# Optimization experiments

Measured on AMD Instinct MI355X. Metric: run time of the kernel, lower is better.

The kernel has to match this reference:

```python
import jax, jax.numpy as jnp
import numpy as np
import math

S, D = 8192, 128

def setup_inputs() -> dict:
    key = jax.random.key(0)
    kq, kk, kv = jax.random.split(key, 3)
    return {
        "q": jax.random.normal(kq, (S, D), dtype=jnp.float32),
        "k": jax.random.normal(kk, (S, D), dtype=jnp.float32),
        "v": jax.random.normal(kv, (S, D), dtype=jnp.float32),
    }

def reference(q, k, v):
    # scores: [S, S]; scale by sqrt(d) as in the torch module
    scale = 1.0 / math.sqrt(q.shape[1])
    scores = (q @ k.T) * scale
    attn = jax.nn.softmax(scores, axis=-1)
    return attn @ v
```

## Files before the change

kernel.cpp:

```cpp
#include <hip/hip_runtime.h>
#include <hip/hip_bf16.h>

#define SEQ 8192
#define HD 128
#define BM 256
#define BN 64
#define NQT (SEQ / BM)
#define THREADS 512

typedef __bf16 bf16_t;
typedef __bf16 bf16x2 __attribute__((ext_vector_type(2)));
typedef __bf16 bf16x8 __attribute__((ext_vector_type(8)));
typedef float f32x4 __attribute__((ext_vector_type(4)));
typedef float f32x16 __attribute__((ext_vector_type(16)));
typedef unsigned int u32x4 __attribute__((ext_vector_type(4)));

#if __has_builtin(__builtin_amdgcn_exp2f)
__device__ inline float exp2_fast(float x) { return __builtin_amdgcn_exp2f(x); }
#else
__device__ inline float exp2_fast(float x) { return exp2f(x); }
#endif

__device__ inline void permswap32(unsigned int& a, unsigned int& b) {
#if __has_builtin(__builtin_amdgcn_permlane32_swap)
  auto r = __builtin_amdgcn_permlane32_swap(a, b, false, false);
  a = (unsigned int)r[0];
  b = (unsigned int)r[1];
#else
  asm volatile("v_permlane32_swap_b32 %0, %1" : "+v"(a), "+v"(b));
#endif
}

__device__ inline void load_lds16(const void* g, void* l) {
  __builtin_amdgcn_global_load_lds(
      (const __attribute__((address_space(1))) void*)g,
      (__attribute__((address_space(3))) void*)l, 16, 0, 0);
}

#define BARRIER(N)                                                         \
  do {                                                                     \
    asm volatile("s_waitcnt vmcnt(" #N ") lgkmcnt(0)\n\ts_barrier" ::: "memory"); \
    __builtin_amdgcn_sched_barrier(0);                                     \
  } while (0)

__global__ __launch_bounds__(256) void prep_kernel(const float* __restrict__ K,
                                                   const float* __restrict__ V,
                                                   bf16_t* __restrict__ Kb,
                                                   bf16_t* __restrict__ VT) {
  const int b = (int)blockIdx.x;
  const int tid = (int)threadIdx.x;
  if (b < 256) {
    __shared__ float tile[64][65];
    const int T = b & 127;
    const int d0 = (b >> 7) * 64;
    const int s0 = T * 64;
    const int r = tid >> 2;
    const int c0 = (tid & 3) * 16;
#pragma unroll
    for (int j4 = 0; j4 < 4; ++j4) {
      float4 x = *(const float4*)&V[(size_t)(s0 + r) * HD + d0 + c0 + j4 * 4];
      tile[r][c0 + j4 * 4 + 0] = x.x;
      tile[r][c0 + j4 * 4 + 1] = x.y;
      tile[r][c0 + j4 * 4 + 2] = x.z;
      tile[r][c0 + j4 * 4 + 3] = x.w;
    }
    __syncthreads();
    const int d_l = tid & 63;
    const int kc0 = (tid >> 6) * 2;
#pragma unroll
    for (int k2 = 0; k2 < 2; ++k2) {
      const int kc = kc0 + k2;
      bf16x8 wv;
#pragma unroll
      for (int j = 0; j < 8; ++j) wv[j] = (bf16_t)tile[kc * 8 + j][d_l];
      *(bf16x8*)&VT[((size_t)(T * 8 + kc) * 128 + d0 + d_l) * 8] = wv;
    }
  } else {
    const int base = (b - 256) * 2048 + tid * 8;
    const int row = base >> 7;
    const int c = (base >> 3) & 15;
    const int T = row >> 6;
    const int r = row & 63;
    float4 a = *(const float4*)&K[base];
    float4 cc = *(const float4*)&K[base + 4];
    bf16x8 f;
    f[0] = (bf16_t)a.x; f[1] = (bf16_t)a.y; f[2] = (bf16_t)a.z; f[3] = (bf16_t)a.w;
    f[4] = (bf16_t)cc.x; f[5] = (bf16_t)cc.y; f[6] = (bf16_t)cc.z; f[7] = (bf16_t)cc.w;
    *(bf16x8*)&Kb[((size_t)(T * 16 + c) * 64 + r) * 8] = f;
  }
}

__global__ __launch_bounds__(THREADS, 2) void fattn_kernel(
    const float* __restrict__ Q, const bf16_t* __restrict__ Kb,
    const bf16_t* __restrict__ VT, float* __restrict__ Opart,
    float* __restrict__ Lpart, int kshift, int nit) {
  __shared__ __align__(16) bf16_t kt3[3][16][64][8];
  __shared__ __align__(16) bf16_t vt3[3][8][128][8];

  const int tid = (int)threadIdx.x;
  const int lane = tid & 63;
  const int w = tid >> 6;
  const int h = lane >> 5;
  const int n32 = lane & 31;

  const int qt = (int)blockIdx.x >> kshift;
  const int sp = (int)blockIdx.x & ((1 << kshift) - 1);
  const int qbase = qt * BM;
  const int tile0 = sp * nit;

  const float SC2 = 0.08838834764831845f * 1.4426950408889634f;

  bf16x8 qf[8];
  {
    const float* qp = Q + (size_t)(qbase + w * 32 + n32) * HD + h * 8;
#pragma unroll
    for (int kk = 0; kk < 8; ++kk) {
      float4 a = *(const float4*)(qp + kk * 16);
      float4 b = *(const float4*)(qp + kk * 16 + 4);
      bf16x8 f;
      f[0] = (bf16_t)(a.x * SC2); f[1] = (bf16_t)(a.y * SC2);
      f[2] = (bf16_t)(a.z * SC2); f[3] = (bf16_t)(a.w * SC2);
      f[4] = (bf16_t)(b.x * SC2); f[5] = (bf16_t)(b.y * SC2);
      f[6] = (bf16_t)(b.z * SC2); f[7] = (bf16_t)(b.w * SC2);
      qf[kk] = f;
    }
  }

  f32x16 o_acc[4];
#pragma unroll
  for (int i = 0; i < 4; ++i)
#pragma unroll
    for (int e = 0; e < 16; ++e) o_acc[i][e] = 0.f;
  float l_acc = 0.f;

  bf16x8 paA[4], paB[4];

  const int rr0 = w * 2;
  char* const ktB = (char*)&kt3[0][0][0][0];
  char* const vtB = (char*)&vt3[0][0][0][0];

#define DMA_K(TILE, BUF)                                                   \
  _Pragma("unroll")                                                        \
  for (int t = 0; t < 2; ++t) {                                            \
    const int rr = rr0 + t;                                                \
    load_lds16(Kb + ((size_t)((TILE) * 16 + rr) * 64 + lane) * 8,          \
               ktB + (BUF) * 16384 + rr * 1024);                           \
  }
#define DMA_V(TILE, BUF)                                                   \
  _Pragma("unroll")                                                        \
  for (int t = 0; t < 2; ++t) {                                            \
    const int rr = rr0 + t;                                                \
    load_lds16(VT + ((size_t)((TILE) * 8 + (rr >> 1)) * 128 + (rr & 1) * 64 + lane) * 8, \
               vtB + (BUF) * 16384 + rr * 1024);                           \
  }

#define EXPPACK1(SACC, KK2, PDST_EXPR)                                     \
  {                                                                        \
    float pf[8];                                                           \
    _Pragma("unroll")                                                      \
    for (int j = 0; j < 8; ++j) pf[j] = exp2_fast((SACC)[8 * (KK2) + j]);  \
    l_acc += ((pf[0] + pf[1]) + (pf[2] + pf[3])) +                         \
             ((pf[4] + pf[5]) + (pf[6] + pf[7]));                          \
    bf16x2 p0, p1, p2, p3;                                                 \
    p0[0] = (bf16_t)pf[0]; p0[1] = (bf16_t)pf[1];                          \
    p1[0] = (bf16_t)pf[2]; p1[1] = (bf16_t)pf[3];                          \
    p2[0] = (bf16_t)pf[4]; p2[1] = (bf16_t)pf[5];                          \
    p3[0] = (bf16_t)pf[6]; p3[1] = (bf16_t)pf[7];                          \
    unsigned int sA = __builtin_bit_cast(unsigned int, p0);                \
    unsigned int sB = __builtin_bit_cast(unsigned int, p1);                \
    unsigned int sC = __builtin_bit_cast(unsigned int, p2);                \
    unsigned int sD = __builtin_bit_cast(unsigned int, p3);                \
    permswap32(sA, sC);                                                    \
    permswap32(sB, sD);                                                    \
    u32x4 fv;                                                              \
    fv[0] = sA; fv[1] = sB; fv[2] = sC; fv[3] = sD;                        \
    (PDST_EXPR) = __builtin_bit_cast(bf16x8, fv);                          \
  }

#define PVC(PP, C)                                                         \
  _Pragma("unroll")                                                        \
  for (int ot = 0; ot < 4; ++ot) {                                         \
    bf16x8 vb = *(const bf16x8*)(vtB + vp * 16384 + ((C) * 2 + h) * 2048 + \
                                 (ot * 32 + n32) * 16);                    \
    o_acc[ot] = __builtin_amdgcn_mfma_f32_32x32x16_bf16(PP[C], vb, o_acc[ot], 0, 0, 0); \
  }

#define FBODY(PPREV, PCUR, DOK, DOV, VMN)                                  \
  {                                                                        \
    if (DOK) { DMA_K(ktile, kd) }                                          \
    if (DOV) { DMA_V(vtile, vd) }                                          \
    f32x16 sacc0, sacc1;                                                   \
    _Pragma("unroll")                                                      \
    for (int e = 0; e < 16; ++e) { sacc0[e] = 0.f; sacc1[e] = 0.f; }       \
    _Pragma("unroll")                                                      \
    for (int kk = 0; kk < 8; ++kk) {                                       \
      bf16x8 af0 = *(const bf16x8*)(ktB + kc * 16384 + (2 * kk + h) * 1024 + n32 * 16); \
      sacc0 = __builtin_amdgcn_mfma_f32_32x32x16_bf16(af0, qf[kk], sacc0, 0, 0, 0); \
      bf16x8 af1 = *(const bf16x8*)(ktB + kc * 16384 + (2 * kk + h) * 1024 + (32 + n32) * 16); \
      sacc1 = __builtin_amdgcn_mfma_f32_32x32x16_bf16(af1, qf[kk], sacc1, 0, 0, 0); \
    }                                                                      \
    PVC(PPREV, 0) EXPPACK1(sacc0, 0, PCUR[0])                              \
    PVC(PPREV, 1) EXPPACK1(sacc0, 1, PCUR[1])                              \
    PVC(PPREV, 2) EXPPACK1(sacc1, 0, PCUR[2])                              \
    PVC(PPREV, 3) EXPPACK1(sacc1, 1, PCUR[3])                              \
    BARRIER(VMN);                                                          \
    kc = (kc + 1 == 3) ? 0 : kc + 1;                                       \
    kd = (kd + 1 == 3) ? 0 : kd + 1;                                       \
    vp = (vp + 1 == 3) ? 0 : vp + 1;                                       \
    vd = (vd + 1 == 3) ? 0 : vd + 1;                                       \
    ++ktile; ++vtile;                                                      \
  }

  DMA_K(tile0, 0)
  DMA_V(tile0, 0)
  DMA_K(tile0 + 1, 1)
  BARRIER(2);

  {
    DMA_K(tile0 + 2, 2)
    DMA_V(tile0 + 1, 1)
    f32x16 sacc0, sacc1;
#pragma unroll
    for (int e = 0; e < 16; ++e) { sacc0[e] = 0.f; sacc1[e] = 0.f; }
#pragma unroll
    for (int kk = 0; kk < 8; ++kk) {
      bf16x8 af0 = *(const bf16x8*)(ktB + (2 * kk + h) * 1024 + n32 * 16);
      sacc0 = __builtin_amdgcn_mfma_f32_32x32x16_bf16(af0, qf[kk], sacc0, 0, 0, 0);
      bf16x8 af1 = *(const bf16x8*)(ktB + (2 * kk + h) * 1024 + (32 + n32) * 16);
      sacc1 = __builtin_amdgcn_mfma_f32_32x32x16_bf16(af1, qf[kk], sacc1, 0, 0, 0);
    }
    EXPPACK1(sacc0, 0, paA[0])
    EXPPACK1(sacc0, 1, paA[1])
    EXPPACK1(sacc1, 0, paA[2])
    EXPPACK1(sacc1, 1, paA[3])
    BARRIER(4);
  }

  int kc = 1, kd = 0;
  int vp = 0, vd = 2;
  int ktile = tile0 + 3;
  int vtile = tile0 + 2;

  for (int it = 1; it <= nit - 4; it += 2) {
    FBODY(paA, paB, 1, 1, 4)
    FBODY(paB, paA, 1, 1, 4)
  }
  FBODY(paA, paB, 1, 1, 4)
  FBODY(paB, paA, 0, 1, 2)
  FBODY(paA, paB, 0, 0, 0)

  PVC(paB, 0)
  PVC(paB, 1)
  PVC(paB, 2)
  PVC(paB, 3)

#undef FBODY
#undef PVC
#undef EXPPACK1
#undef DMA_K
#undef DMA_V

  {
    float* op = Opart + ((size_t)sp * SEQ + qbase + w * 32) * HD;
#pragma unroll
    for (int ot = 0; ot < 4; ++ot)
#pragma unroll
      for (int reg = 0; reg < 16; ++reg) {
        const int row = (reg & 3) + 8 * (reg >> 2) + 4 * h;
        op[row * HD + ot * 32 + n32] = o_acc[ot][reg];
      }
    float l = l_acc + __shfl_xor(l_acc, 32);
    if (lane < 32)
      Lpart[(size_t)sp * SEQ + qbase + w * 32 + n32] = l;
  }
}

__global__ __launch_bounds__(256) void combine_kernel(const float* __restrict__ Opart,
                                                      const float* __restrict__ Lpart,
                                                      float* __restrict__ out, int ksplit) {
  const int tid = (int)threadIdx.x;
  const int row = (int)blockIdx.x * 8 + (tid >> 5);
  const int c0 = (tid & 31) * 4;
  float lsum = 0.f;
  for (int s = 0; s < ksplit; ++s) lsum += Lpart[(size_t)s * SEQ + row];
  f32x4 acc;
#pragma unroll
  for (int e = 0; e < 4; ++e) acc[e] = 0.f;
  for (int s = 0; s < ksplit; ++s) {
    f32x4 o = *(const f32x4*)&Opart[((size_t)s * SEQ + row) * HD + c0];
#pragma unroll
    for (int e = 0; e < 4; ++e) acc[e] += o[e];
  }
  const float inv = 1.0f / lsum;
  f32x4 res;
#pragma unroll
  for (int e = 0; e < 4; ++e) res[e] = acc[e] * inv;
  *(f32x4*)&out[(size_t)row * HD + c0] = res;
}

extern "C" void kernel_launch(void* const* d_in, const int* in_sizes, int n_in,
                              void* d_out, int out_size, void* d_ws, size_t ws_size,
                              hipStream_t stream) {
  const float* Q = (const float*)d_in[0];
  const float* K = (const float*)d_in[1];
  const float* V = (const float*)d_in[2];
  float* out = (float*)d_out;

  int ksplit = 8, kshift = 3;
  while (ksplit > 1) {
    size_t need = (size_t)ksplit * SEQ * HD * 4
                + (size_t)ksplit * SEQ * 4
                + (size_t)SEQ * HD * 2 * 2;
    if (need <= ws_size) break;
    ksplit >>= 1; kshift--;
  }

  char* ws = (char*)d_ws;
  float* Opart = (float*)ws;
  float* Lpart = (float*)(ws + (size_t)ksplit * SEQ * HD * 4);
  bf16_t* Kb = (bf16_t*)(ws + (size_t)ksplit * SEQ * HD * 4 + (size_t)ksplit * SEQ * 4);
  bf16_t* VT = Kb + (size_t)SEQ * HD;

  const int nit = SEQ / (ksplit * BN);

  prep_kernel<<<768, 256, 0, stream>>>(K, V, Kb, VT);
  fattn_kernel<<<NQT * ksplit, THREADS, 0, stream>>>(Q, Kb, VT, Opart, Lpart, kshift, nit);
  combine_kernel<<<SEQ / 8, 256, 0, stream>>>(Opart, Lpart, out, ksplit);
}
```

Baseline: 110.7 us.

## Split attention loop body into barrier-separated load and MFMA phases with priority

Restructures the main loop body into four phases. In each phase the K or V fragments are first loaded from LDS into registers, then the workgroup synchronises and a burst of MFMAs runs under raised wave priority (s_setprio). This aims to keep waves in lockstep, so that one wave's LDS reads overlap other waves' matrix math and MFMA bursts run back to back. It adds several extra barriers per iteration, needs more registers to hold the fragment arrays, and moves the exp/pack work away from being interleaved with the PV MFMAs.

```diff
diff --git a/kernel.cpp b/kernel.cpp
--- a/kernel.cpp
+++ b/kernel.cpp
@@ -42,6 +42,14 @@
     asm volatile("s_waitcnt vmcnt(" #N ") lgkmcnt(0)\n\ts_barrier" ::: "memory"); \
     __builtin_amdgcn_sched_barrier(0);                                     \
   } while (0)
+
+#define PH()                                                               \
+  do {                                                                     \
+    __builtin_amdgcn_s_barrier();                                          \
+    asm volatile("s_waitcnt lgkmcnt(0)" ::: "memory");                     \
+    __builtin_amdgcn_sched_barrier(0);                                     \
+  } while (0)
+#define PB() __builtin_amdgcn_s_barrier()
 
 __global__ __launch_bounds__(256) void prep_kernel(const float* __restrict__ K,
                                                    const float* __restrict__ V,
@@ -187,22 +195,70 @@
 
 #define FBODY(PPREV, PCUR, DOK, DOV, VMN)                                  \
   {                                                                        \
+    f32x16 sacc0, sacc1;                                                   \
+    _Pragma("unroll")                                                      \
+    for (int e = 0; e < 16; ++e) { sacc0[e] = 0.f; sacc1[e] = 0.f; }       \
+      \
     if (DOK) { DMA_K(ktile, kd) }                                          \
     if (DOV) { DMA_V(vtile, vd) }                                          \
-    f32x16 sacc0, sacc1;                                                   \
-    _Pragma("unroll")                                                      \
-    for (int e = 0; e < 16; ++e) { sacc0[e] = 0.f; sacc1[e] = 0.f; }       \
-    _Pragma("unroll")                                                      \
-    for (int kk = 0; kk < 8; ++kk) {                                       \
-      bf16x8 af0 = *(const bf16x8*)(ktB + kc * 16384 + (2 * kk + h) * 1024 + n32 * 16); \
-      sacc0 = __builtin_amdgcn_mfma_f32_32x32x16_bf16(af0, qf[kk], sacc0, 0, 0, 0); \
-      bf16x8 af1 = *(const bf16x8*)(ktB + kc * 16384 + (2 * kk + h) * 1024 + (32 + n32) * 16); \
-      sacc1 = __builtin_amdgcn_mfma_f32_32x32x16_bf16(af1, qf[kk], sacc1, 0, 0, 0); \
-    }                                                                      \
-    PVC(PPREV, 0) EXPPACK1(sacc0, 0, PCUR[0])                              \
-    PVC(PPREV, 1) EXPPACK1(sacc0, 1, PCUR[1])                              \
-    PVC(PPREV, 2) EXPPACK1(sacc1, 0, PCUR[2])                              \
-    PVC(PPREV, 3) EXPPACK1(sacc1, 1, PCUR[3])                              \
+    bf16x8 af[8];                                                          \
+    _Pragma("unroll")                                                      \
+    for (int kk = 0; kk < 8; ++kk)                                         \
+      af[kk] = *(const bf16x8*)(ktB + kc * 16384 + (2 * kk + h) * 1024 + n32 * 16); \
+    PH();                                                                  \
+    __builtin_amdgcn_s_setprio(1);                                         \
+    _Pragma("unroll")                                                      \
+    for (int kk = 0; kk < 8; ++kk)                                         \
+      sacc0 = __builtin_amdgcn_mfma_f32_32x32x16_bf16(af[kk], qf[kk], sacc0, 0, 0, 0); \
+    __builtin_amdgcn_s_setprio(0);                                         \
+    PB();                                                                  \
+                 \
+    _Pragma("unroll")                                                      \
+    for (int kk = 0; kk < 8; ++kk)                                         \
+      af[kk] = *(const bf16x8*)(ktB + kc * 16384 + (2 * kk + h) * 1024 + (32 + n32) * 16); \
+    PH();                                                                  \
+    __builtin_amdgcn_s_setprio(1);                                         \
+    _Pragma("unroll")                                                      \
+    for (int kk = 0; kk < 8; ++kk)                                         \
+      sacc1 = __builtin_amdgcn_mfma_f32_32x32x16_bf16(af[kk], qf[kk], sacc1, 0, 0, 0); \
+    __builtin_amdgcn_s_setprio(0);                                         \
+    PB();                                                                  \
+         \
+    bf16x8 vb[8];                                                          \
+    _Pragma("unroll")                                                      \
+    for (int C = 0; C < 2; ++C)                                            \
+      _Pragma("unroll")                                                    \
+      for (int ot = 0; ot < 4; ++ot)                                       \
+        vb[C * 4 + ot] = *(const bf16x8*)(vtB + vp * 16384 + (C * 2 + h) * 2048 + \
+                                          (ot * 32 + n32) * 16);           \
+    EXPPACK1(sacc0, 0, PCUR[0])                                            \
+    EXPPACK1(sacc0, 1, PCUR[1])                                            \
+    PH();                                                                  \
+    __builtin_amdgcn_s_setprio(1);                                         \
+    _Pragma("unroll")                                                      \
+    for (int C = 0; C < 2; ++C)                                            \
+      _Pragma("unroll")                                                    \
+      for (int ot = 0; ot < 4; ++ot)                                       \
+        o_acc[ot] = __builtin_amdgcn_mfma_f32_32x32x16_bf16(PPREV[C], vb[C * 4 + ot], o_acc[ot], 0, 0, 0); \
+    __builtin_amdgcn_s_setprio(0);                                         \
+    PB();                                                                  \
+         \
+    _Pragma("unroll")                                                      \
+    for (int C = 0; C < 2; ++C)                                            \
+      _Pragma("unroll")                                                    \
+      for (int ot = 0; ot < 4; ++ot)                                       \
+        vb[C * 4 + ot] = *(const bf16x8*)(vtB + vp * 16384 + ((C + 2) * 2 + h) * 2048 + \
+                                          (ot * 32 + n32) * 16);           \
+    EXPPACK1(sacc1, 0, PCUR[2])                                            \
+    EXPPACK1(sacc1, 1, PCUR[3])                                            \
+    PH();                                                                  \
+    __builtin_amdgcn_s_setprio(1);                                         \
+    _Pragma("unroll")                                                      \
+    for (int C = 0; C < 2; ++C)                                            \
+      _Pragma("unroll")                                                    \
+      for (int ot = 0; ot < 4; ++ot)                                       \
+        o_acc[ot] = __builtin_amdgcn_mfma_f32_32x32x16_bf16(PPREV[C + 2], vb[C * 4 + ot], o_acc[ot], 0, 0, 0); \
+    __builtin_amdgcn_s_setprio(0);                                         \
     BARRIER(VMN);                                                          \
     kc = (kc + 1 == 3) ? 0 : kc + 1;                                       \
     kd = (kd + 1 == 3) ? 0 : kd + 1;                                       \
```

New measurement: 115.9 us. 1.05x slower.

## Warp-specialize attention into QK/softmax and PV wave groups via LDS

Applied to the files above, without the earlier changes.

Doubles the block to 1024 threads and splits the waves into two roles: eight waves compute QK^T and the exponentials, writing bf16 P tiles into a double-buffered LDS buffer, while the other eight load V and run the PV MFMAs. K/V buffering drops from triple to double and every step ends with a full vmcnt(0) barrier. The aim is to overlap the softmax and PV phases on separate waves and lower per-wave register pressure. In exchange it adds LDS traffic for P, more barriers and a lockstep dependency between the groups, and the launch bound of 4 blocks of 1024 threads per CU may not be satisfiable.

```diff
diff --git a/kernel.cpp b/kernel.cpp
--- a/kernel.cpp
+++ b/kernel.cpp
@@ -6,7 +6,7 @@
 #define BM 256
 #define BN 64
 #define NQT (SEQ / BM)
-#define THREADS 512
+#define THREADS 1024
 
 typedef __bf16 bf16_t;
 typedef __bf16 bf16x2 __attribute__((ext_vector_type(2)));
@@ -37,9 +37,9 @@
       (__attribute__((address_space(3))) void*)l, 16, 0, 0);
 }
 
-#define BARRIER(N)                                                         \
+#define SYNC()                                                             \
   do {                                                                     \
-    asm volatile("s_waitcnt vmcnt(" #N ") lgkmcnt(0)\n\ts_barrier" ::: "memory"); \
+    asm volatile("s_waitcnt vmcnt(0) lgkmcnt(0)\n\ts_barrier" ::: "memory"); \
     __builtin_amdgcn_sched_barrier(0);                                     \
   } while (0)
 
@@ -90,16 +90,18 @@
   }
 }
 
-__global__ __launch_bounds__(THREADS, 2) void fattn_kernel(
+__global__ __launch_bounds__(THREADS, 4) void fattn_kernel(
     const float* __restrict__ Q, const bf16_t* __restrict__ Kb,
     const bf16_t* __restrict__ VT, float* __restrict__ Opart,
     float* __restrict__ Lpart, int kshift, int nit) {
-  __shared__ __align__(16) bf16_t kt3[3][16][64][8];
-  __shared__ __align__(16) bf16_t vt3[3][8][128][8];
+  __shared__ __align__(16) bf16_t kt2[2][16][64][8];
+  __shared__ __align__(16) bf16_t vt2[2][8][128][8];
+  __shared__ __align__(16) char pbuf[2][8][4][64][16];
 
   const int tid = (int)threadIdx.x;
   const int lane = tid & 63;
   const int w = tid >> 6;
+  const int qw = w & 7;
   const int h = lane >> 5;
   const int n32 = lane & 31;
 
@@ -110,51 +112,26 @@
 
   const float SC2 = 0.08838834764831845f * 1.4426950408889634f;
 
-  bf16x8 qf[8];
-  {
-    const float* qp = Q + (size_t)(qbase + w * 32 + n32) * HD + h * 8;
-#pragma unroll
-    for (int kk = 0; kk < 8; ++kk) {
-      float4 a = *(const float4*)(qp + kk * 16);
-      float4 b = *(const float4*)(qp + kk * 16 + 4);
-      bf16x8 f;
-      f[0] = (bf16_t)(a.x * SC2); f[1] = (bf16_t)(a.y * SC2);
-      f[2] = (bf16_t)(a.z * SC2); f[3] = (bf16_t)(a.w * SC2);
-      f[4] = (bf16_t)(b.x * SC2); f[5] = (bf16_t)(b.y * SC2);
-      f[6] = (bf16_t)(b.z * SC2); f[7] = (bf16_t)(b.w * SC2);
-      qf[kk] = f;
-    }
-  }
-
-  f32x16 o_acc[4];
-#pragma unroll
-  for (int i = 0; i < 4; ++i)
-#pragma unroll
-    for (int e = 0; e < 16; ++e) o_acc[i][e] = 0.f;
-  float l_acc = 0.f;
-
-  bf16x8 paA[4], paB[4];
-
-  const int rr0 = w * 2;
-  char* const ktB = (char*)&kt3[0][0][0][0];
-  char* const vtB = (char*)&vt3[0][0][0][0];
+  char* const ktB = (char*)&kt2[0][0][0][0];
+  char* const vtB = (char*)&vt2[0][0][0][0];
+  char* const pbB = (char*)&pbuf[0][0][0][0][0];
 
 #define DMA_K(TILE, BUF)                                                   \
   _Pragma("unroll")                                                        \
   for (int t = 0; t < 2; ++t) {                                            \
-    const int rr = rr0 + t;                                                \
+    const int rr = qw * 2 + t;                                             \
     load_lds16(Kb + ((size_t)((TILE) * 16 + rr) * 64 + lane) * 8,          \
                ktB + (BUF) * 16384 + rr * 1024);                           \
   }
 #define DMA_V(TILE, BUF)                                                   \
   _Pragma("unroll")                                                        \
   for (int t = 0; t < 2; ++t) {                                            \
-    const int rr = rr0 + t;                                                \
+    const int rr = qw * 2 + t;                                             \
     load_lds16(VT + ((size_t)((TILE) * 8 + (rr >> 1)) * 128 + (rr & 1) * 64 + lane) * 8, \
                vtB + (BUF) * 16384 + rr * 1024);                           \
   }
 
-#define EXPPACK1(SACC, KK2, PDST_EXPR)                                     \
+#define EXPPACKW(SACC, KK2, CIDX, BUF)                                     \
   {                                                                        \
     float pf[8];                                                           \
     _Pragma("unroll")                                                      \
@@ -174,94 +151,97 @@
     permswap32(sB, sD);                                                    \
     u32x4 fv;                                                              \
     fv[0] = sA; fv[1] = sB; fv[2] = sC; fv[3] = sD;                        \
-    (PDST_EXPR) = __builtin_bit_cast(bf16x8, fv);                          \
-  }
-
-#define PVC(PP, C)                                                         \
-  _Pragma("unroll")                                                        \
-  for (int ot = 0; ot < 4; ++ot) {                                         \
-    bf16x8 vb = *(const bf16x8*)(vtB + vp * 16384 + ((C) * 2 + h) * 2048 + \
-                                 (ot * 32 + n32) * 16);                    \
-    o_acc[ot] = __builtin_amdgcn_mfma_f32_32x32x16_bf16(PP[C], vb, o_acc[ot], 0, 0, 0); \
-  }
-
-#define FBODY(PPREV, PCUR, DOK, DOV, VMN)                                  \
+    *(u32x4*)(pbB + (BUF) * 32768 + qw * 4096 + (CIDX) * 1024 + lane * 16) = fv; \
+  }
+
+#define QKBODY(IT, CUR)                                                    \
   {                                                                        \
-    if (DOK) { DMA_K(ktile, kd) }                                          \
-    if (DOV) { DMA_V(vtile, vd) }                                          \
+    const int it_ = (IT);                                                  \
+    if (it_ + 1 < nit) { DMA_K(tile0 + it_ + 1, (CUR) ^ 1) }               \
     f32x16 sacc0, sacc1;                                                   \
     _Pragma("unroll")                                                      \
     for (int e = 0; e < 16; ++e) { sacc0[e] = 0.f; sacc1[e] = 0.f; }       \
     _Pragma("unroll")                                                      \
     for (int kk = 0; kk < 8; ++kk) {                                       \
-      bf16x8 af0 = *(const bf16x8*)(ktB + kc * 16384 + (2 * kk + h) * 1024 + n32 * 16); \
+      bf16x8 af0 = *(const bf16x8*)(ktB + (CUR) * 16384 + (2 * kk + h) * 1024 + n32 * 16); \
       sacc0 = __builtin_amdgcn_mfma_f32_32x32x16_bf16(af0, qf[kk], sacc0, 0, 0, 0); \
-      bf16x8 af1 = *(const bf16x8*)(ktB + kc * 16384 + (2 * kk + h) * 1024 + (32 + n32) * 16); \
+      bf16x8 af1 = *(const bf16x8*)(ktB + (CUR) * 16384 + (2 * kk + h) * 1024 + (32 + n32) * 16); \
       sacc1 = __builtin_amdgcn_mfma_f32_32x32x16_bf16(af1, qf[kk], sacc1, 0, 0, 0); \
     }                                                                      \
-    PVC(PPREV, 0) EXPPACK1(sacc0, 0, PCUR[0])                              \
-    PVC(PPREV, 1) EXPPACK1(sacc0, 1, PCUR[1])                              \
-    PVC(PPREV, 2) EXPPACK1(sacc1, 0, PCUR[2])                              \
-    PVC(PPREV, 3) EXPPACK1(sacc1, 1, PCUR[3])                              \
-    BARRIER(VMN);                                                          \
-    kc = (kc + 1 == 3) ? 0 : kc + 1;                                       \
-    kd = (kd + 1 == 3) ? 0 : kd + 1;                                       \
-    vp = (vp + 1 == 3) ? 0 : vp + 1;                                       \
-    vd = (vd + 1 == 3) ? 0 : vd + 1;                                       \
-    ++ktile; ++vtile;                                                      \
-  }
-
-  DMA_K(tile0, 0)
-  DMA_V(tile0, 0)
-  DMA_K(tile0 + 1, 1)
-  BARRIER(2);
-
-  {
-    DMA_K(tile0 + 2, 2)
-    DMA_V(tile0 + 1, 1)
-    f32x16 sacc0, sacc1;
-#pragma unroll
-    for (int e = 0; e < 16; ++e) { sacc0[e] = 0.f; sacc1[e] = 0.f; }
-#pragma unroll
-    for (int kk = 0; kk < 8; ++kk) {
-      bf16x8 af0 = *(const bf16x8*)(ktB + (2 * kk + h) * 1024 + n32 * 16);
-      sacc0 = __builtin_amdgcn_mfma_f32_32x32x16_bf16(af0, qf[kk], sacc0, 0, 0, 0);
-      bf16x8 af1 = *(const bf16x8*)(ktB + (2 * kk + h) * 1024 + (32 + n32) * 16);
-      sacc1 = __builtin_amdgcn_mfma_f32_32x32x16_bf16(af1, qf[kk], sacc1, 0, 0, 0);
-    }
-    EXPPACK1(sacc0, 0, paA[0])
-    EXPPACK1(sacc0, 1, paA[1])
-    EXPPACK1(sacc1, 0, paA[2])
-    EXPPACK1(sacc1, 1, paA[3])
-    BARRIER(4);
-  }
-
-  int kc = 1, kd = 0;
-  int vp = 0, vd = 2;
-  int ktile = tile0 + 3;
-  int vtile = tile0 + 2;
-
-  for (int it = 1; it <= nit - 4; it += 2) {
-    FBODY(paA, paB, 1, 1, 4)
-    FBODY(paB, paA, 1, 1, 4)
-  }
-  FBODY(paA, paB, 1, 1, 4)
-  FBODY(paB, paA, 0, 1, 2)
-  FBODY(paA, paB, 0, 0, 0)
-
-  PVC(paB, 0)
-  PVC(paB, 1)
-  PVC(paB, 2)
-  PVC(paB, 3)
-
-#undef FBODY
-#undef PVC
-#undef EXPPACK1
-#undef DMA_K
-#undef DMA_V
-
-  {
-    float* op = Opart + ((size_t)sp * SEQ + qbase + w * 32) * HD;
+    EXPPACKW(sacc0, 0, 0, CUR)                                             \
+    EXPPACKW(sacc0, 1, 1, CUR)                                             \
+    EXPPACKW(sacc1, 0, 2, CUR)                                             \
+    EXPPACKW(sacc1, 1, 3, CUR)                                             \
+    SYNC();                                                                \
+  }
+
+#define PVCOMP(PBUF)                                                       \
+  _Pragma("unroll")                                                        \
+  for (int C = 0; C < 4; ++C) {                                            \
+    bf16x8 pa = *(const bf16x8*)(pbB + (PBUF) * 32768 + qw * 4096 + C * 1024 + lane * 16); \
+    _Pragma("unroll")                                                      \
+    for (int ot = 0; ot < 4; ++ot) {                                       \
+      bf16x8 vb = *(const bf16x8*)(vtB + (PBUF) * 16384 + (C * 2 + h) * 2048 + \
+                                   (ot * 32 + n32) * 16);                  \
+      o_acc[ot] = __builtin_amdgcn_mfma_f32_32x32x16_bf16(pa, vb, o_acc[ot], 0, 0, 0); \
+    }                                                                      \
+  }
+
+#define PVBODY(IT, CUR)                                                    \
+  {                                                                        \
+    DMA_V(tile0 + (IT), CUR)                                               \
+    PVCOMP((CUR) ^ 1)                                                      \
+    SYNC();                                                                \
+  }
+
+  if (w < 8) {
+    bf16x8 qf[8];
+    {
+      const float* qp = Q + (size_t)(qbase + qw * 32 + n32) * HD + h * 8;
+#pragma unroll
+      for (int kk = 0; kk < 8; ++kk) {
+        float4 a = *(const float4*)(qp + kk * 16);
+        float4 b = *(const float4*)(qp + kk * 16 + 4);
+        bf16x8 f;
+        f[0] = (bf16_t)(a.x * SC2); f[1] = (bf16_t)(a.y * SC2);
+        f[2] = (bf16_t)(a.z * SC2); f[3] = (bf16_t)(a.w * SC2);
+        f[4] = (bf16_t)(b.x * SC2); f[5] = (bf16_t)(b.y * SC2);
+        f[6] = (bf16_t)(b.z * SC2); f[7] = (bf16_t)(b.w * SC2);
+        qf[kk] = f;
+      }
+    }
+    float l_acc = 0.f;
+
+    DMA_K(tile0, 0)
+    SYNC();
+
+    for (int it = 0; it < nit; it += 2) {
+      QKBODY(it, 0)
+      QKBODY(it + 1, 1)
+    }
+
+    float l = l_acc + __shfl_xor(l_acc, 32);
+    if (lane < 32)
+      Lpart[(size_t)sp * SEQ + qbase + qw * 32 + n32] = l;
+  } else {
+    f32x16 o_acc[4];
+#pragma unroll
+    for (int i = 0; i < 4; ++i)
+#pragma unroll
+      for (int e = 0; e < 16; ++e) o_acc[i][e] = 0.f;
+
+    SYNC();
+
+    DMA_V(tile0, 0)
+    SYNC();
+    PVBODY(1, 1)
+    for (int it = 2; it < nit; it += 2) {
+      PVBODY(it, 0)
+      PVBODY(it + 1, 1)
+    }
+    PVCOMP(1)
+
+    float* op = Opart + ((size_t)sp * SEQ + qbase + qw * 32) * HD;
 #pragma unroll
     for (int ot = 0; ot < 4; ++ot)
 #pragma unroll
@@ -269,10 +249,14 @@
         const int row = (reg & 3) + 8 * (reg >> 2) + 4 * h;
         op[row * HD + ot * 32 + n32] = o_acc[ot][reg];
       }
-    float l = l_acc + __shfl_xor(l_acc, 32);
-    if (lane < 32)
-      Lpart[(size_t)sp * SEQ + qbase + w * 32 + n32] = l;
-  }
+  }
+
+#undef QKBODY
+#undef PVBODY
+#undef PVCOMP
+#undef EXPPACKW
+#undef DMA_K
+#undef DMA_V
 }
 
 __global__ __launch_bounds__(256) void combine_kernel(const float* __restrict__ Opart,
```

New measurement: 108.6 us. About the same (-1.9%).
